# Performance work log

Measured on AMD Instinct MI355X. Metric: run time of the kernel, lower is better.

## Reference

```python
import jax, jax.numpy as jnp
import numpy as np

B, S, D, H, L = 2, 2048, 768, 12, 12
DH = D // H
REL_POS_BINS, MAX_REL_POS = 32, 128
REL_2D_POS_BINS, MAX_REL_2D_POS = 64, 256
LN_EPS = 1e-12


def setup_inputs() -> dict:
    key = jax.random.key(0)
    ks = jax.random.split(key, 12)
    s = 0.02
    return {
        "hidden_states": jax.random.normal(ks[0], (B, S, D), jnp.float32),
        "attention_mask": jnp.zeros((B, 1, 1, S), jnp.bool_),  # True = masked
        "position_ids": jnp.sort(jax.random.randint(ks[1], (B, S), 0, 1024), axis=-1),
        "bbox": jax.random.randint(ks[2], (B, S, 4), 0, 1024),
        # stacked per-layer params (torch Linear applied as x @ W + b)
        "q_w": jax.random.normal(ks[3], (L, D, D), jnp.float32) * s,
        "q_b": jnp.zeros((L, D), jnp.float32),
        "k_w": jax.random.normal(ks[4], (L, D, D), jnp.float32) * s,
        "k_b": jnp.zeros((L, D), jnp.float32),
        "v_w": jax.random.normal(ks[5], (L, D, D), jnp.float32) * s,
        "v_b": jnp.zeros((L, D), jnp.float32),
        "o_w": jax.random.normal(ks[6], (L, D, D), jnp.float32) * s,
        "o_b": jnp.zeros((L, D), jnp.float32),
        "ln_g": jnp.ones((L, D), jnp.float32),
        "ln_b": jnp.zeros((L, D), jnp.float32),
        # rel-pos bias heads x buckets (nn.Linear(bins, heads, bias=False).weight)
        "rel_pos_bias_w": jax.random.normal(ks[7], (H, REL_POS_BINS), jnp.float32) * s,
        "rel_x_bias_w": jax.random.normal(ks[8], (H, REL_2D_POS_BINS), jnp.float32) * s,
        "rel_y_bias_w": jax.random.normal(ks[9], (H, REL_2D_POS_BINS), jnp.float32) * s,
    }


def _rel_bucket(rel, num_buckets, max_distance):
    # bidirectional bucketing from Mesh-TF / ErnieLayout
    nb = num_buckets // 2
    ret = (rel > 0).astype(jnp.int32) * nb
    n = jnp.abs(rel).astype(jnp.int32)
    max_exact = nb // 2
    is_small = n < max_exact
    nf = jnp.maximum(n, 1).astype(jnp.float32)  # avoid log(0); masked by is_small
    val_large = max_exact + (
        jnp.log(nf / max_exact) / np.log(max_distance / max_exact) * (nb - max_exact)
    ).astype(jnp.int32)
    val_large = jnp.minimum(val_large, nb - 1)
    return ret + jnp.where(is_small, n, val_large)


def _bias_from_table(ids_1d, table, num_buckets, max_distance):
    # ids_1d: [B,S] int; table: [H, buckets] -> bias [B,H,S,S]
    rel = ids_1d[:, None, :] - ids_1d[:, :, None]  # memory - query
    buckets = _rel_bucket(rel, num_buckets, max_distance)  # [B,S,S]
    return jnp.transpose(table.T[buckets], (0, 3, 1, 2))  # one-hot @ W.T == gather


def _layer_norm(x, g, b):
    m = jnp.mean(x, axis=-1, keepdims=True)
    v = jnp.mean((x - m) ** 2, axis=-1, keepdims=True)
    return (x - m) / jnp.sqrt(v + LN_EPS) * g + b


def reference(hidden_states, attention_mask, position_ids, bbox,
              q_w, q_b, k_w, k_b, v_w, v_b, o_w, o_b, ln_g, ln_b,
              rel_pos_bias_w, rel_x_bias_w, rel_y_bias_w):
    rel_pos = _bias_from_table(position_ids, rel_pos_bias_w, REL_POS_BINS, MAX_REL_POS)
    rel_2d = (_bias_from_table(bbox[:, :, 0], rel_x_bias_w, REL_2D_POS_BINS, MAX_REL_2D_POS)
              + _bias_from_table(bbox[:, :, 3], rel_y_bias_w, REL_2D_POS_BINS, MAX_REL_2D_POS))
    bias = rel_pos + rel_2d  # [B,H,S,S], shared across layers
    neg = jnp.finfo(jnp.float32).min
    inv_sqrt_dh = 1.0 / np.sqrt(DH)

    def layer(h, p):
        qw, qb, kw, kb, vw, vb, ow, ob, g, bb = p
        q = (h @ qw + qb).reshape(B, S, H, DH).transpose(0, 2, 1, 3) * inv_sqrt_dh
        k = (h @ kw + kb).reshape(B, S, H, DH).transpose(0, 2, 1, 3)
        v = (h @ vw + vb).reshape(B, S, H, DH).transpose(0, 2, 1, 3)
        scores = jnp.einsum('bhqd,bhkd->bhqk', q, k) + bias
        scores = jnp.where(attention_mask, neg, scores)
        probs = jax.nn.softmax(scores, axis=-1)
        ctx = jnp.einsum('bhqk,bhkd->bhqd', probs, v).transpose(0, 2, 1, 3).reshape(B, S, D)
        out = ctx @ ow + ob  # ErnieLayoutSelfOutput dense
        return _layer_norm(out + h, g, bb), None

    h, _ = jax.lax.scan(layer, hidden_states,
                        (q_w, q_b, k_w, k_b, v_w, v_b, o_w, o_b, ln_g, ln_b))
    return h
```

## Files before the change

kernel.cpp:

```cpp
#include <hip/hip_runtime.h>


#define BB 2
#define SS 2048
#define DD 768
#define HH 12
#define NLAYER 12
#define MM 4096

typedef unsigned short u16;
typedef unsigned char u8;
typedef __attribute__((ext_vector_type(8))) short bf16x8;
typedef __attribute__((ext_vector_type(4))) float f32x4;
typedef __attribute__((ext_vector_type(2))) float f32x2;

#define LOG2E 1.44269504088896340736f
#define WT_LSTRIDE 2359296

__device__ __forceinline__ u16 f2bf(float f) {
  unsigned u = __float_as_uint(f);
  unsigned r = (u + 0x7FFFu + ((u >> 16) & 1u)) >> 16;
  return (u16)r;
}
__device__ __forceinline__ float bf2f(unsigned u) {
  return __uint_as_float(u << 16);
}
__device__ __forceinline__ unsigned cvtpk(float a, float b) {
  unsigned r;
  asm("v_cvt_pk_bf16_f32 %0, %1, %2" : "=v"(r) : "v"(a), "v"(b));
  return r;
}
__device__ __forceinline__ float exp2v(float x) {
  float r;
  asm("v_exp_f32 %0, %1" : "=v"(r) : "v"(x));
  return r;
}
__device__ __forceinline__ float log2v(float x) {
  float r;
  asm("v_log_f32 %0, %1" : "=v"(r) : "v"(x));
  return r;
}
__device__ __forceinline__ float max3f(float a, float b, float c) {
  float r;
  asm("v_max3_f32 %0, %1, %2, %3" : "=v"(r) : "v"(a), "v"(b), "v"(c));
  return r;
}

__device__ __forceinline__ void g2lds16(const void* g, void* l) {
  __builtin_amdgcn_global_load_lds(
      (const __attribute__((address_space(1))) unsigned int*)g,
      (__attribute__((address_space(3))) unsigned int*)l, 16, 0, 0);
}

__global__ __launch_bounds__(256) void k_hb(const float4* __restrict__ x,
                                            uint2* __restrict__ o, int n4) {
  int i = blockIdx.x * 256 + threadIdx.x;
  if (i < n4) {
    float4 v = x[i];
    uint2 r;
    r.x = (unsigned)f2bf(v.x) | ((unsigned)f2bf(v.y) << 16);
    r.y = (unsigned)f2bf(v.z) | ((unsigned)f2bf(v.w) << 16);
    o[i] = r;
  }
}

__device__ __forceinline__ int bucket1(int rel) {
  int ret = rel > 0 ? 16 : 0;
  int n = rel < 0 ? -rel : rel;
  if (n < 8) return ret + n;
  int v = 8 + (int)(log2v((float)n * 0.125f) * 2.0f);
  return ret + (v < 15 ? v : 15);
}
__device__ __forceinline__ int bucket2(int rel) {
  int ret = rel > 0 ? 32 : 0;
  int n = rel < 0 ? -rel : rel;
  if (n < 16) return ret + n;
  int v = 16 + (int)(log2v((float)n * 0.0625f) * 4.0f);
  return ret + (v < 31 ? v : 31);
}

__global__ __launch_bounds__(256) void k_bias(
    const int* __restrict__ pos, const int* __restrict__ bbx,
    const unsigned char* __restrict__ msk,
    const float* __restrict__ wp, const float* __restrict__ wx,
    const float* __restrict__ wy, u8* __restrict__ bias) {
  int bid = blockIdx.x;
  int b = bid >> 10, qt = (bid >> 5) & 31, kt = bid & 31;
  __shared__ __align__(16) float swpT[3][32][4], swxT[3][64][4], swyT[3][64][4];
  __shared__ int pq[64], xq[64], yq[64], pk[64], xk[64], yk[64];
  __shared__ unsigned char mk[64];
  int t = threadIdx.x;
  for (int i = t; i < 384; i += 256) {
    int g = i >> 7, idx = i & 127;
    swpT[g][idx >> 2][idx & 3] = wp[(g * 4 + (idx & 3)) * 32 + (idx >> 2)] * LOG2E;
  }
  for (int i = t; i < 768; i += 256) {
    int g = i >> 8, idx = i & 255;
    swxT[g][idx >> 2][idx & 3] = wx[(g * 4 + (idx & 3)) * 64 + (idx >> 2)] * LOG2E;
    swyT[g][idx >> 2][idx & 3] = wy[(g * 4 + (idx & 3)) * 64 + (idx >> 2)] * LOG2E;
  }
  int q0 = qt * 64, k0 = kt * 64;
  if (t < 64) {
    int gi = b * SS + q0 + t;
    pq[t] = pos[gi]; xq[t] = bbx[gi * 4]; yq[t] = bbx[gi * 4 + 3];
  } else if (t < 128) {
    int j = t - 64, gi = b * SS + k0 + j;
    pk[j] = pos[gi]; xk[j] = bbx[gi * 4]; yk[j] = bbx[gi * 4 + 3];
    mk[j] = msk[b * SS + k0 + j];
  }
  __syncthreads();
  int w = t >> 6, l = t & 63;
  int hi = l >> 4;
  int qlr = w * 16 + (l & 15);
  int pql = pq[qlr], xql = xq[qlr], yql = yq[qlr];
  int packed[16];
#pragma unroll
  for (int fn = 0; fn < 4; fn++)
#pragma unroll
    for (int r = 0; r < 4; r++) {
      int kl = fn * 16 + hi * 4 + r;
      int b1 = bucket1(pk[kl] - pql);
      int b2 = bucket2(xk[kl] - xql);
      int b3 = bucket2(yk[kl] - yql);
      packed[fn * 4 + r] = b1 | (b2 << 5) | (b3 << 11) | (mk[kl] ? (1 << 17) : 0);
    }
  for (int hg = 0; hg < 3; hg++) {
    unsigned words[4][4];
#pragma unroll
    for (int j2 = 0; j2 < 8; j2++) {
      float a0[4], a1[4];
      {
        int p = packed[2 * j2];
        f32x4 ap = *(const f32x4*)swpT[hg][p & 31];
        f32x4 bx = *(const f32x4*)swxT[hg][(p >> 5) & 63];
        f32x4 cy = *(const f32x4*)swyT[hg][(p >> 11) & 63];
        bool mm = (p >> 17) != 0;
#pragma unroll
        for (int hh = 0; hh < 4; hh++)
          a0[hh] = mm ? -3.0e38f : (ap[hh] + bx[hh] + cy[hh]);
      }
      {
        int p = packed[2 * j2 + 1];
        f32x4 ap = *(const f32x4*)swpT[hg][p & 31];
        f32x4 bx = *(const f32x4*)swxT[hg][(p >> 5) & 63];
        f32x4 cy = *(const f32x4*)swyT[hg][(p >> 11) & 63];
        bool mm = (p >> 17) != 0;
#pragma unroll
        for (int hh = 0; hh < 4; hh++)
          a1[hh] = mm ? -3.0e38f : (ap[hh] + bx[hh] + cy[hh]);
      }
      int wd = j2 >> 1;
      if ((j2 & 1) == 0) {
#pragma unroll
        for (int hh = 0; hh < 4; hh++)
          words[hh][wd] = __builtin_amdgcn_cvt_pk_fp8_f32(a0[hh], a1[hh], 0, false);
      } else {
#pragma unroll
        for (int hh = 0; hh < 4; hh++)
          words[hh][wd] = __builtin_amdgcn_cvt_pk_fp8_f32(a0[hh], a1[hh],
                                                          words[hh][wd], true);
      }
    }
#pragma unroll
    for (int hh = 0; hh < 4; hh++) {
      int h = hg * 4 + hh;
      u8* dst = bias +
          ((size_t)((b * 12 + h) * 1024 + qt * 32 + kt) * 256 + t) * 16;
      *(uint4*)dst = make_uint4(words[hh][0], words[hh][1], words[hh][2],
                                words[hh][3]);
    }
  }
}

__global__ __launch_bounds__(256) void k_wconv_all(
    const float* __restrict__ qw, const float* __restrict__ kw,
    const float* __restrict__ vw, const float* __restrict__ ow,
    u16* __restrict__ wt) {
  int bid = blockIdx.x;
  int layer = bid / 576, rem = bid % 576;
  int g = rem / 144, rr_ = rem % 144, nt = rr_ / 12, kt = rr_ % 12;
  const float* src = g == 0 ? qw : g == 1 ? kw : g == 2 ? vw : ow;
  src += (size_t)layer * DD * DD;
  __shared__ float sm[64][67];
  int t = threadIdx.x, c2 = t & 31, r0 = t >> 5;
#pragma unroll
  for (int p = 0; p < 8; p++) {
    int row = r0 + p * 8;
    float2 v = *(const float2*)&src[(size_t)(kt * 64 + row) * DD + nt * 64 + c2 * 2];
    sm[row][c2 * 2] = v.x;
    sm[row][c2 * 2 + 1] = v.y;
  }
  __syncthreads();
  u16* dst = wt + (size_t)layer * WT_LSTRIDE + (size_t)g * DD * DD;
#pragma unroll
  for (int p = 0; p < 8; p++) {
    int n = r0 + p * 8;
    float v0 = sm[c2 * 2][n], v1 = sm[c2 * 2 + 1][n];
    *(unsigned*)&dst[(size_t)(nt * 64 + n) * DD + kt * 64 + c2 * 2] = cvtpk(v0, v1);
  }
}

__device__ __forceinline__ void gemm_core(const u16* __restrict__ A,
                                          const u16* __restrict__ Bt, u16* As,
                                          u16* Bs, f32x4 acc[4][4], int tid) {
  int w = tid >> 6, l = tid & 63;
  int wm = w >> 1, wn = w & 1;
#pragma unroll
  for (int i = 0; i < 4; i++)
#pragma unroll
    for (int j = 0; j < 4; j++) acc[i][j] = f32x4{0.f, 0.f, 0.f, 0.f};
  for (int kt = 0; kt < 12; kt++) {
    __syncthreads();
    int r0 = w * 32;
#pragma unroll
    for (int j = 0; j < 4; j++) {
      int row = r0 + j * 8 + (l >> 3);
      int sl = (l & 7) ^ (row & 7);
      g2lds16(A + (size_t)row * DD + kt * 64 + sl * 8, As + (r0 + j * 8) * 64);
      g2lds16(Bt + (size_t)row * DD + kt * 64 + sl * 8, Bs + (r0 + j * 8) * 64);
    }
    __syncthreads();
#pragma unroll
    for (int kk = 0; kk < 2; kk++) {
      bf16x8 af[4], bfr[4];
#pragma unroll
      for (int fm = 0; fm < 4; fm++) {
        int row = wm * 64 + fm * 16 + (l & 15);
        int slot = (kk * 4 + (l >> 4)) ^ (row & 7);
        af[fm] = *(const bf16x8*)((const char*)As + row * 128 + slot * 16);
      }
#pragma unroll
      for (int fn = 0; fn < 4; fn++) {
        int row = wn * 64 + fn * 16 + (l & 15);
        int slot = (kk * 4 + (l >> 4)) ^ (row & 7);
        bfr[fn] = *(const bf16x8*)((const char*)Bs + row * 128 + slot * 16);
      }
#pragma unroll
      for (int fm = 0; fm < 4; fm++)
#pragma unroll
        for (int fn = 0; fn < 4; fn++)
          acc[fm][fn] = __builtin_amdgcn_mfma_f32_16x16x32_bf16(
              af[fm], bfr[fn], acc[fm][fn], 0, 0, 0);
    }
  }
}

__global__ __launch_bounds__(256) void k_gemm_qkv(
    const u16* __restrict__ hb, const u16* __restrict__ wt,
    const float* __restrict__ qbias, const float* __restrict__ kbias,
    const float* __restrict__ vbias, u16* __restrict__ qo, u16* __restrict__ ko,
    u16* __restrict__ vtb) {
  __shared__ __align__(16) u16 As[128 * 64];
  __shared__ __align__(16) u16 Bs[128 * 64];
  int bid0 = blockIdx.x;
  int bid = (bid0 & 7) * 72 + (bid0 >> 3);
  int mblk = bid / 18, nblk = bid % 18;
  int g = nblk / 6, nb = nblk % 6;
  const u16* A = hb + (size_t)mblk * 128 * DD;
  const u16* Bt = wt + (size_t)g * DD * DD + (size_t)nb * 128 * DD;
  f32x4 acc[4][4];
  gemm_core(A, Bt, As, Bs, acc, threadIdx.x);
  int w = threadIdx.x >> 6, l = threadIdx.x & 63;
  int wm = w >> 1, wn = w & 1;
  int hi4 = (l >> 4) << 2;
  if (g == 2) {
#pragma unroll
    for (int fn = 0; fn < 4; fn++) {
      int col = nb * 128 + wn * 64 + fn * 16 + (l & 15);
      float bval = vbias[col];
      int h = col >> 6, d = col & 63;
#pragma unroll
      for (int fm = 0; fm < 4; fm++) {
        int row = mblk * 128 + wm * 64 + fm * 16 + hi4;
        int bb = row >> 11, s = row & 2047;
        unsigned p0 = cvtpk(acc[fm][fn][0] + bval, acc[fm][fn][1] + bval);
        unsigned p1 = cvtpk(acc[fm][fn][2] + bval, acc[fm][fn][3] + bval);
        *(uint2*)(vtb + ((size_t)(bb * 12 + h) * 64 + d) * 2048 + s) =
            make_uint2(p0, p1);
      }
    }
    return;
  }
  const float* bias = g == 0 ? qbias : kbias;
  u16* out = g == 0 ? qo : ko;
  float scale = g == 0 ? 0.125f * LOG2E : 1.0f;
#pragma unroll
  for (int fn = 0; fn < 4; fn++) {
    int col = nb * 128 + wn * 64 + fn * 16 + (l & 15);
    float bval = bias[col];
#pragma unroll
    for (int fm = 0; fm < 4; fm++)
#pragma unroll
      for (int r = 0; r < 4; r++) {
        int row = mblk * 128 + wm * 64 + fm * 16 + hi4 + r;
        out[(size_t)row * DD + col] = f2bf((acc[fm][fn][r] + bval) * scale);
      }
  }
}

__global__ __launch_bounds__(256) void k_gemm_o(const u16* __restrict__ ctx,
                                                const u16* __restrict__ wto,
                                                const float* __restrict__ obias,
                                                u16* __restrict__ outp) {
  __shared__ __align__(16) u16 As[128 * 64];
  __shared__ __align__(16) u16 Bs[128 * 64];
  int bid0 = blockIdx.x;
  int bid = (bid0 & 7) * 24 + (bid0 >> 3);
  int mblk = bid / 6, nblk = bid % 6;
  const u16* A = ctx + (size_t)mblk * 128 * DD;
  const u16* Bt = wto + (size_t)nblk * 128 * DD;
  f32x4 acc[4][4];
  gemm_core(A, Bt, As, Bs, acc, threadIdx.x);
  int w = threadIdx.x >> 6, l = threadIdx.x & 63;
  int wm = w >> 1, wn = w & 1;
#pragma unroll
  for (int fn = 0; fn < 4; fn++) {
    int col = nblk * 128 + wn * 64 + fn * 16 + (l & 15);
    float bval = obias[col];
#pragma unroll
    for (int fm = 0; fm < 4; fm++)
#pragma unroll
      for (int r = 0; r < 4; r++) {
        int row = mblk * 128 + wm * 64 + fm * 16 + ((l >> 4) << 2) + r;
        outp[(size_t)row * DD + col] = f2bf(acc[fm][fn][r] + bval);
      }
  }
}

__global__ __launch_bounds__(256) void k_attn(
    const u16* __restrict__ qm, const u16* __restrict__ kmat,
    const u16* __restrict__ vt, const u8* __restrict__ bias,
    u16* __restrict__ ctx) {
  int bid0 = blockIdx.x;
  int bid = (bid0 & 7) * 96 + (bid0 >> 3);
  int qt = bid & 31, bh = bid >> 5;
  int b = bh / 12, h = bh % 12;
  __shared__ __align__(16) u16 Ks[2][64 * 64];
  __shared__ __align__(16) u16 Vs[2][64 * 64];
  __shared__ __align__(16) u16 Ps[4][16 * 64];
  int tid = threadIdx.x, w = tid >> 6, l = tid & 63;
  int hi = l >> 4, qr = l & 15;
  int q0 = qt * 64;
  const u16* qp = qm + (size_t)(b * SS + q0 + w * 16 + qr) * DD + h * 64 +
                  hi * 8;
  bf16x8 aq0 = *(const bf16x8*)qp;
  bf16x8 aq1 = *(const bf16x8*)(qp + 32);
  const u16* kb_ = kmat + (size_t)(b * SS) * DD + h * 64;
  const u16* vb_ = vt + (size_t)bh * 64 * SS;
  const u8* bb_ = bias + ((size_t)(bh * 32 + qt) * 32 * 256 + tid) * 16;
  f32x4 oa[4];
#pragma unroll
  for (int fn = 0; fn < 4; fn++) oa[fn] = f32x4{0.f, 0.f, 0.f, 0.f};
  f32x4 lacc = f32x4{0.f, 0.f, 0.f, 0.f};
  float m_ = -3.0e38f;
  bf16x8 vones;
#pragma unroll
  for (int i = 0; i < 8; i++) vones[i] = (short)0x3F80;
  int srow = tid >> 3, sc8 = tid & 7;

  auto STAGE = [&](int kt, int buf) {
#pragma unroll
    for (int j = 0; j < 2; j++) {
      int rr = srow + j * 32;
      int sl = sc8 ^ (rr & 7);
      g2lds16(kb_ + (size_t)(kt * 64 + rr) * DD + sl * 8,
              &Ks[buf][tid * 8 + j * 2048]);
      g2lds16(vb_ + (size_t)rr * SS + kt * 64 + sl * 8,
              &Vs[buf][tid * 8 + j * 2048]);
    }
  };

  STAGE(0, 0);
  uint4 bu = *(const uint4*)bb_;
  uint4 nb = bu;
  char* pw = (char*)&Ps[w][0] + qr * 128;
  int qs = (qr & 7) << 4;
  __syncthreads();

  for (int kt = 0; kt < 32; kt++) {
    int buf = kt & 1;
    if (kt < 31) {
      STAGE(kt + 1, buf ^ 1);
      nb = *(const uint4*)(bb_ + (size_t)(kt + 1) * 4096);
    }
    f32x4 sc[4];
    {
      unsigned uw[4] = {bu.x, bu.y, bu.z, bu.w};
#pragma unroll
      for (int fn = 0; fn < 4; fn++) {
        f32x2 p0 = __builtin_amdgcn_cvt_pk_f32_fp8(uw[fn], false);
        f32x2 p1 = __builtin_amdgcn_cvt_pk_f32_fp8(uw[fn], true);
        sc[fn][0] = p0.x; sc[fn][1] = p0.y; sc[fn][2] = p1.x; sc[fn][3] = p1.y;
      }
    }
    __builtin_amdgcn_s_setprio(1);
#pragma unroll
    for (int kk = 0; kk < 2; kk++) {
      bf16x8 aq = kk == 0 ? aq0 : aq1;
#pragma unroll
      for (int fn = 0; fn < 4; fn++) {
        int row = fn * 16 + qr;
        int slot = (kk * 4 + hi) ^ (row & 7);
        bf16x8 bk = *(const bf16x8*)((const char*)&Ks[buf][0] + row * 128 +
                                     slot * 16);
        sc[fn] = __builtin_amdgcn_mfma_f32_16x16x32_bf16(bk, aq, sc[fn],
                                                         0, 0, 0);
      }
    }
    __builtin_amdgcn_s_setprio(0);
    float pa = max3f(sc[0][0], sc[0][1], sc[0][2]);
    float pb = max3f(sc[0][3], sc[1][0], sc[1][1]);
    pa = max3f(pa, sc[1][2], sc[1][3]);
    pb = max3f(pb, sc[2][0], sc[2][1]);
    pa = max3f(pa, sc[2][2], sc[2][3]);
    pb = max3f(pb, sc[3][0], sc[3][1]);
    pa = max3f(pa, sc[3][2], sc[3][3]);
    float pm = fmaxf(pa, pb);
    pm = fmaxf(pm, __shfl_xor(pm, 16));
    pm = fmaxf(pm, __shfl_xor(pm, 32));
    if (__any(pm > m_ + 8.f)) {
      float mn = fmaxf(m_, pm);
      float f = exp2v(m_ - mn);
#pragma unroll
      for (int fn = 0; fn < 4; fn++)
#pragma unroll
        for (int r = 0; r < 4; r++) oa[fn][r] *= f;
#pragma unroll
      for (int r = 0; r < 4; r++) lacc[r] *= f;
      m_ = mn;
    }
#pragma unroll
    for (int fn = 0; fn < 4; fn++)
#pragma unroll
      for (int r = 0; r < 4; r++) sc[fn][r] = exp2v(sc[fn][r] - m_);
#pragma unroll
    for (int fn = 0; fn < 4; fn++) {
      unsigned w0 = cvtpk(sc[fn][0], sc[fn][1]);
      unsigned w1 = cvtpk(sc[fn][2], sc[fn][3]);
      *(uint2*)(pw + ((fn * 32 + hi * 8) ^ qs)) = make_uint2(w0, w1);
    }
    __builtin_amdgcn_s_setprio(1);
#pragma unroll
    for (int ck = 0; ck < 2; ck++) {
      bf16x8 pt = *(const bf16x8*)(pw + ((ck * 64 + hi * 16) ^ qs));
#pragma unroll
      for (int fn = 0; fn < 4; fn++) {
        int row = fn * 16 + qr;
        int slot = (ck * 4 + hi) ^ (row & 7);
        bf16x8 av = *(const bf16x8*)((const char*)&Vs[buf][0] + row * 128 +
                                     slot * 16);
        oa[fn] = __builtin_amdgcn_mfma_f32_16x16x32_bf16(av, pt, oa[fn],
                                                         0, 0, 0);
      }
      lacc = __builtin_amdgcn_mfma_f32_16x16x32_bf16(vones, pt, lacc, 0, 0, 0);
    }
    __builtin_amdgcn_s_setprio(0);
    bu = nb;
    __syncthreads();
  }
  float inv = 1.0f / lacc[0];
  u16* cp = ctx + (size_t)(b * SS + q0 + w * 16 + qr) * DD + h * 64 + hi * 4;
#pragma unroll
  for (int fn = 0; fn < 4; fn++) {
    unsigned w0 = cvtpk(oa[fn][0] * inv, oa[fn][1] * inv);
    unsigned w1 = cvtpk(oa[fn][2] * inv, oa[fn][3] * inv);
    *(uint2*)(cp + fn * 16) = make_uint2(w0, w1);
  }
}

__global__ __launch_bounds__(256) void k_ln(const u16* __restrict__ x,
                                            const float* __restrict__ res,
                                            const float* __restrict__ g,
                                            const float* __restrict__ bta,
                                            float* __restrict__ ho,
                                            u16* __restrict__ hbo) {
  int w = threadIdx.x >> 6, l = threadIdx.x & 63;
  int row = blockIdx.x * 4 + w;
  const u16* xr = x + (size_t)row * DD;
  const float* rr = res + (size_t)row * DD;
  float v[12];
  float s = 0.f, s2 = 0.f;
#pragma unroll
  for (int j = 0; j < 3; j++) {
    int c = j * 256 + l * 4;
    uint2 xv = *(const uint2*)(xr + c);
    float4 rv = *(const float4*)(rr + c);
    float a0 = bf2f(xv.x & 0xffffu) + rv.x;
    float a1 = bf2f(xv.x >> 16) + rv.y;
    float a2 = bf2f(xv.y & 0xffffu) + rv.z;
    float a3 = bf2f(xv.y >> 16) + rv.w;
    v[j * 4 + 0] = a0; v[j * 4 + 1] = a1; v[j * 4 + 2] = a2; v[j * 4 + 3] = a3;
    s += (a0 + a1) + (a2 + a3);
    s2 += (a0 * a0 + a1 * a1) + (a2 * a2 + a3 * a3);
  }
#pragma unroll
  for (int m = 1; m < 64; m <<= 1) {
    s += __shfl_xor(s, m);
    s2 += __shfl_xor(s2, m);
  }
  float mean = s * (1.f / 768.f);
  float var = s2 * (1.f / 768.f) - mean * mean;
  float rstd = rsqrtf(var + 1e-12f);
#pragma unroll
  for (int j = 0; j < 3; j++) {
    int c = j * 256 + l * 4;
    float4 gv = *(const float4*)(g + c);
    float4 bv = *(const float4*)(bta + c);
    float y0 = (v[j * 4 + 0] - mean) * rstd * gv.x + bv.x;
    float y1 = (v[j * 4 + 1] - mean) * rstd * gv.y + bv.y;
    float y2 = (v[j * 4 + 2] - mean) * rstd * gv.z + bv.z;
    float y3 = (v[j * 4 + 3] - mean) * rstd * gv.w + bv.w;
    *(float4*)(ho + (size_t)row * DD + c) = make_float4(y0, y1, y2, y3);
    *(uint2*)(hbo + (size_t)row * DD + c) =
        make_uint2(cvtpk(y0, y1), cvtpk(y2, y3));
  }
}

extern "C" void kernel_launch(void* const* d_in, const int* in_sizes, int n_in,
                              void* d_out, int out_size, void* d_ws,
                              size_t ws_size, hipStream_t stream) {
  const float* hid = (const float*)d_in[0];
  const unsigned char* msk = (const unsigned char*)d_in[1];
  const int* pos = (const int*)d_in[2];
  const int* bbx = (const int*)d_in[3];
  const float* qw = (const float*)d_in[4];
  const float* qbv = (const float*)d_in[5];
  const float* kw = (const float*)d_in[6];
  const float* kbv = (const float*)d_in[7];
  const float* vw = (const float*)d_in[8];
  const float* vbv = (const float*)d_in[9];
  const float* ow = (const float*)d_in[10];
  const float* obv = (const float*)d_in[11];
  const float* lng = (const float*)d_in[12];
  const float* lnb = (const float*)d_in[13];
  const float* wpb = (const float*)d_in[14];
  const float* wxb = (const float*)d_in[15];
  const float* wyb = (const float*)d_in[16];
  float* outp = (float*)d_out;

  char* p = (char*)d_ws;
  u8* bias = (u8*)p;     p += (size_t)100663296;
  float* hbuf = (float*)p; p += 12582912;
  u16* hb = (u16*)p;     p += 6291456;
  u16* qo = (u16*)p;     p += 6291456;
  u16* ko = (u16*)p;     p += 6291456;
  u16* vtb = (u16*)p;    p += 6291456;
  u16* ctxb = (u16*)p;   p += 6291456;
  u16* wtb = (u16*)p;    p += (size_t)56623104;
  u16* att = qo;

  k_hb<<<dim3(3072), dim3(256), 0, stream>>>((const float4*)hid, (uint2*)hb,
                                             786432);
  k_bias<<<dim3(2048), dim3(256), 0, stream>>>(pos, bbx, msk, wpb, wxb, wyb,
                                               bias);
  k_wconv_all<<<dim3(6912), dim3(256), 0, stream>>>(qw, kw, vw, ow, wtb);
  for (int l = 0; l < NLAYER; l++) {
    const u16* wl = wtb + (size_t)l * WT_LSTRIDE;
    k_gemm_qkv<<<dim3(576), dim3(256), 0, stream>>>(
        hb, wl, qbv + l * DD, kbv + l * DD, vbv + l * DD, qo, ko, vtb);
    k_attn<<<dim3(768), dim3(256), 0, stream>>>(qo, ko, vtb, bias, ctxb);
    k_gemm_o<<<dim3(192), dim3(256), 0, stream>>>(
        ctxb, wl + (size_t)3 * DD * DD, obv + l * DD, att);
    k_ln<<<dim3(1024), dim3(256), 0, stream>>>(
        att, l == 0 ? hid : (const float*)hbuf, lng + l * DD, lnb + l * DD,
        l == 11 ? outp : hbuf, hb);
  }
}
```

Before: 1.409 ms.

## Double-buffer GEMM LDS tiles and load V fragments directly from global in attention

```diff
diff --git a/kernel.cpp b/kernel.cpp
--- a/kernel.cpp
+++ b/kernel.cpp
@@ -209,17 +209,25 @@
   for (int i = 0; i < 4; i++)
 #pragma unroll
     for (int j = 0; j < 4; j++) acc[i][j] = f32x4{0.f, 0.f, 0.f, 0.f};
-  for (int kt = 0; kt < 12; kt++) {
-    __syncthreads();
-    int r0 = w * 32;
+  int r0 = w * 32;
+  auto STG = [&](int kt, int buf) {
 #pragma unroll
     for (int j = 0; j < 4; j++) {
       int row = r0 + j * 8 + (l >> 3);
       int sl = (l & 7) ^ (row & 7);
-      g2lds16(A + (size_t)row * DD + kt * 64 + sl * 8, As + (r0 + j * 8) * 64);
-      g2lds16(Bt + (size_t)row * DD + kt * 64 + sl * 8, Bs + (r0 + j * 8) * 64);
-    }
-    __syncthreads();
+      g2lds16(A + (size_t)row * DD + kt * 64 + sl * 8,
+              As + buf * 8192 + (r0 + j * 8) * 64);
+      g2lds16(Bt + (size_t)row * DD + kt * 64 + sl * 8,
+              Bs + buf * 8192 + (r0 + j * 8) * 64);
+    }
+  };
+  STG(0, 0);
+  __syncthreads();
+  for (int kt = 0; kt < 12; kt++) {
+    int buf = kt & 1;
+    if (kt < 11) STG(kt + 1, buf ^ 1);
+    const char* Ab = (const char*)(As + buf * 8192);
+    const char* Bb = (const char*)(Bs + buf * 8192);
 #pragma unroll
     for (int kk = 0; kk < 2; kk++) {
       bf16x8 af[4], bfr[4];
@@ -227,13 +235,13 @@
       for (int fm = 0; fm < 4; fm++) {
         int row = wm * 64 + fm * 16 + (l & 15);
         int slot = (kk * 4 + (l >> 4)) ^ (row & 7);
-        af[fm] = *(const bf16x8*)((const char*)As + row * 128 + slot * 16);
+        af[fm] = *(const bf16x8*)(Ab + row * 128 + slot * 16);
       }
 #pragma unroll
       for (int fn = 0; fn < 4; fn++) {
         int row = wn * 64 + fn * 16 + (l & 15);
         int slot = (kk * 4 + (l >> 4)) ^ (row & 7);
-        bfr[fn] = *(const bf16x8*)((const char*)Bs + row * 128 + slot * 16);
+        bfr[fn] = *(const bf16x8*)(Bb + row * 128 + slot * 16);
       }
 #pragma unroll
       for (int fm = 0; fm < 4; fm++)
@@ -242,6 +250,7 @@
           acc[fm][fn] = __builtin_amdgcn_mfma_f32_16x16x32_bf16(
               af[fm], bfr[fn], acc[fm][fn], 0, 0, 0);
     }
+    __syncthreads();
   }
 }
 
@@ -250,8 +259,8 @@
     const float* __restrict__ qbias, const float* __restrict__ kbias,
     const float* __restrict__ vbias, u16* __restrict__ qo, u16* __restrict__ ko,
     u16* __restrict__ vtb) {
-  __shared__ __align__(16) u16 As[128 * 64];
-  __shared__ __align__(16) u16 Bs[128 * 64];
+  __shared__ __align__(16) u16 As[2 * 128 * 64];
+  __shared__ __align__(16) u16 Bs[2 * 128 * 64];
   int bid0 = blockIdx.x;
   int bid = (bid0 & 7) * 72 + (bid0 >> 3);
   int mblk = bid / 18, nblk = bid % 18;
@@ -302,8 +311,8 @@
                                                 const u16* __restrict__ wto,
                                                 const float* __restrict__ obias,
                                                 u16* __restrict__ outp) {
-  __shared__ __align__(16) u16 As[128 * 64];
-  __shared__ __align__(16) u16 Bs[128 * 64];
+  __shared__ __align__(16) u16 As[2 * 128 * 64];
+  __shared__ __align__(16) u16 Bs[2 * 128 * 64];
   int bid0 = blockIdx.x;
   int bid = (bid0 & 7) * 24 + (bid0 >> 3);
   int mblk = bid / 6, nblk = bid % 6;
@@ -336,7 +345,6 @@
   int qt = bid & 31, bh = bid >> 5;
   int b = bh / 12, h = bh % 12;
   __shared__ __align__(16) u16 Ks[2][64 * 64];
-  __shared__ __align__(16) u16 Vs[2][64 * 64];
   __shared__ __align__(16) u16 Ps[4][16 * 64];
   int tid = threadIdx.x, w = tid >> 6, l = tid & 63;
   int hi = l >> 4, qr = l & 15;
@@ -347,6 +355,7 @@
   bf16x8 aq1 = *(const bf16x8*)(qp + 32);
   const u16* kb_ = kmat + (size_t)(b * SS) * DD + h * 64;
   const u16* vb_ = vt + (size_t)bh * 64 * SS;
+  const u16* vL = vb_ + (size_t)qr * SS + hi * 8;
   const u8* bb_ = bias + ((size_t)(bh * 32 + qt) * 32 * 256 + tid) * 16;
   f32x4 oa[4];
 #pragma unroll
@@ -365,8 +374,6 @@
       int sl = sc8 ^ (rr & 7);
       g2lds16(kb_ + (size_t)(kt * 64 + rr) * DD + sl * 8,
               &Ks[buf][tid * 8 + j * 2048]);
-      g2lds16(vb_ + (size_t)rr * SS + kt * 64 + sl * 8,
-              &Vs[buf][tid * 8 + j * 2048]);
     }
   };
 
@@ -379,6 +386,13 @@
 
   for (int kt = 0; kt < 32; kt++) {
     int buf = kt & 1;
+    bf16x8 cv[8];
+#pragma unroll
+    for (int ck = 0; ck < 2; ck++)
+#pragma unroll
+      for (int fn = 0; fn < 4; fn++)
+        cv[ck * 4 + fn] = *(const bf16x8*)(vL + (size_t)fn * 16 * SS +
+                                           kt * 64 + ck * 32);
     if (kt < 31) {
       STAGE(kt + 1, buf ^ 1);
       nb = *(const uint4*)(bb_ + (size_t)(kt + 1) * 4096);
@@ -444,14 +458,9 @@
     for (int ck = 0; ck < 2; ck++) {
       bf16x8 pt = *(const bf16x8*)(pw + ((ck * 64 + hi * 16) ^ qs));
 #pragma unroll
-      for (int fn = 0; fn < 4; fn++) {
-        int row = fn * 16 + qr;
-        int slot = (ck * 4 + hi) ^ (row & 7);
-        bf16x8 av = *(const bf16x8*)((const char*)&Vs[buf][0] + row * 128 +
-                                     slot * 16);
-        oa[fn] = __builtin_amdgcn_mfma_f32_16x16x32_bf16(av, pt, oa[fn],
-                                                         0, 0, 0);
-      }
+      for (int fn = 0; fn < 4; fn++)
+        oa[fn] = __builtin_amdgcn_mfma_f32_16x16x32_bf16(cv[ck * 4 + fn], pt,
+                                                         oa[fn], 0, 0, 0);
       lacc = __builtin_amdgcn_mfma_f32_16x16x32_bf16(vones, pt, lacc, 0, 0, 0);
     }
     __builtin_amdgcn_s_setprio(0);
```

After: 1.950 ms. 38.4% more time.
